# Kernel optimization log

Hardware: AMD Instinct MI355X
Metric: run time of the kernel (lower is better)

Reference implementation:

```python
import jax, jax.numpy as jnp
import numpy as np

D_LATENT = 8
N_CENTERS = 48
CHANNELS = 64
PM_STEPS = 4
DT, BETA, CLAMP = 0.12, 1.0, 3.0
SIGMA_E, SIGMA_I, K_E, K_I, GAIN = 0.6, 1.2, 0.8, 1.0, 0.06


def setup_inputs() -> dict:
    key = jax.random.key(0)
    ks = jax.random.split(key, 12)
    B = 8192
    x = jax.random.normal(ks[0], (B, 784), dtype=jnp.float32)
    # encoder params (torch Linear default-ish init scale)
    W1 = jax.random.normal(ks[1], (784, 256), dtype=jnp.float32) * (1.0 / np.sqrt(784))
    b1 = jnp.zeros((256,), jnp.float32)
    W2 = jax.random.normal(ks[2], (256, D_LATENT), dtype=jnp.float32) * (1.0 / np.sqrt(256))
    b2 = jnp.zeros((D_LATENT,), jnp.float32)
    centers = jax.random.normal(ks[3], (N_CENTERS, D_LATENT), dtype=jnp.float32) * 0.7
    mus = jnp.ones((N_CENTERS,), jnp.float32) * 0.4
    projW = jax.random.normal(ks[4], (D_LATENT, CHANNELS), dtype=jnp.float32) * (1.0 / np.sqrt(D_LATENT))
    projb = jnp.zeros((CHANNELS,), jnp.float32)
    roW = jax.random.normal(ks[5], (CHANNELS, 10), dtype=jnp.float32) * (1.0 / np.sqrt(CHANNELS))
    rob = jnp.zeros((10,), jnp.float32)
    return {"x": x, "W1": W1, "b1": b1, "W2": W2, "b2": b2,
            "centers": centers, "mus": mus, "projW": projW, "projb": projb,
            "roW": roW, "rob": rob, "T": 5}


def _pm_field(z, centers, mus):
    # one PMField forward: `PM_STEPS` gradient-flow steps on z [B, d]
    for _ in range(PM_STEPS):
        diff = z[:, None, :] - centers[None, :, :]            # [B, C, d]
        r2 = jnp.sum(diff * diff, axis=-1) + 1e-4              # [B, C]
        r = jnp.sqrt(r2)
        n = 1.0 + jnp.sum(mus[None, :] / r, axis=1)            # [B]
        g = -jnp.sum(mus[None, :, None] * diff / (r * r2)[:, :, None], axis=1)  # [B, d]
        z = z + DT * BETA * (g / n[:, None])
        z = jnp.clip(z, -CLAMP, CLAMP)
    return z


def _lateral_ei(z, h):
    # kernel computed with no_grad in torch -> stop_gradient here
    sq = jnp.sum(z * z, axis=1)                                # [B]
    dist2 = jnp.maximum(sq[:, None] + sq[None, :] - 2.0 * (z @ z.T), 0.0)
    Ke = K_E * jnp.exp(-dist2 / (2.0 * SIGMA_E ** 2))
    Ki = K_I * jnp.exp(-dist2 / (2.0 * SIGMA_I ** 2))
    K = Ke - Ki
    K = K / (jnp.sum(K, axis=1, keepdims=True) + 1e-6)
    K = jax.lax.stop_gradient(K)
    return GAIN * (K @ h)


def reference(x, W1, b1, W2, b2, centers, mus, projW, projb, roW, rob, T):
    z = jnp.tanh(x @ W1 + b1) @ W2 + b2                        # encoder -> [B, d]
    h = jnp.zeros((x.shape[0], CHANNELS), x.dtype)
    logits = None
    for _ in range(T):
        z = _pm_field(z, centers, mus)
        h = 0.9 * h + 0.1 * jnp.tanh(z @ projW + projb)
        h = h + _lateral_ei(z, h)
        logits = h @ roW + rob
    return logits, z, h
```

## Files before the change

kernel.cpp:

```cpp
#include <hip/hip_runtime.h>
#include <hip/hip_bf16.h>
#include <math.h>

#define B_N      8192
#define IN_DIM   784
#define HID      256
#define DL       8
#define NC       48
#define CH       64
#define NCLS     10
#define T_ITERS  5
#define TILES    128

#define DT_      0.12f
#define CLAMP_   3.0f
#define GAIN_    0.06f
#define SQIL2    0.70776814f
#define ONE_BF16 0x3F80u

#if defined(__has_builtin)
#if __has_builtin(__builtin_amdgcn_exp2f)
#define EXP2(x) __builtin_amdgcn_exp2f(x)
#endif
#endif
#ifndef EXP2
#define EXP2(x) exp2f(x)
#endif

typedef __attribute__((ext_vector_type(8))) short short8v;
typedef __attribute__((ext_vector_type(4))) float f32x4;

__device__ __forceinline__ unsigned int pack_bf16_rhu(float lo, float hi) {
    unsigned int b0 = __builtin_bit_cast(unsigned int, lo);
    unsigned int b1 = __builtin_bit_cast(unsigned int, hi);
    return ((b0 + 0x8000u) >> 16) | ((b1 + 0x8000u) & 0xFFFF0000u);
}
__device__ __forceinline__ unsigned short bf16_1(float x) {
    return (unsigned short)((__builtin_bit_cast(unsigned int, x) + 0x8000u) >> 16);
}
__device__ __forceinline__ float bf16_to_f(unsigned short h) {
    return __builtin_bit_cast(float, ((unsigned int)h) << 16);
}

__global__ __launch_bounds__(256) void k_gemm1_tanh(
    const float* __restrict__ x, const float* __restrict__ W1,
    const float* __restrict__ b1, float* __restrict__ H1)
{
    __shared__ float As[16][68];
    __shared__ float Bs[16][64];
    const int tid = threadIdx.x;
    const int row0 = blockIdx.x * 64;
    const int col0 = blockIdx.y * 64;
    const int tr = tid >> 4, tc = tid & 15;
    float acc[4][4] = {};
    for (int k0 = 0; k0 < IN_DIM; k0 += 16) {
        {
            int m = tid >> 2, kq = tid & 3;
            float4 v = *(const float4*)(x + (size_t)(row0 + m) * IN_DIM + k0 + kq * 4);
            As[kq*4+0][m] = v.x; As[kq*4+1][m] = v.y;
            As[kq*4+2][m] = v.z; As[kq*4+3][m] = v.w;
        }
        {
            int kk = tid >> 4, n4 = tid & 15;
            *(float4*)(&Bs[kk][n4*4]) =
                *(const float4*)(W1 + (size_t)(k0 + kk) * HID + col0 + n4 * 4);
        }
        __syncthreads();
        #pragma unroll
        for (int kk = 0; kk < 16; ++kk) {
            float4 a = *(const float4*)(&As[kk][tr*4]);
            float4 b = *(const float4*)(&Bs[kk][tc*4]);
            float av[4] = {a.x, a.y, a.z, a.w};
            float bv[4] = {b.x, b.y, b.z, b.w};
            #pragma unroll
            for (int i = 0; i < 4; ++i)
                #pragma unroll
                for (int j = 0; j < 4; ++j)
                    acc[i][j] += av[i] * bv[j];
        }
        __syncthreads();
    }
    #pragma unroll
    for (int i = 0; i < 4; ++i) {
        int r = row0 + tr*4 + i;
        #pragma unroll
        for (int j = 0; j < 4; ++j) {
            int c = col0 + tc*4 + j;
            H1[(size_t)r * HID + c] = tanhf(acc[i][j] + b1[c]);
        }
    }
}

__global__ __launch_bounds__(256) void k_gemm2(
    const float* __restrict__ H1, const float* __restrict__ W2,
    const float* __restrict__ b2, float* __restrict__ zbuf)
{
    __shared__ float W2s[HID][DL];
    const int tid = threadIdx.x;
    for (int l = tid; l < HID * DL; l += 256) W2s[l >> 3][l & 7] = W2[l];
    __syncthreads();
    const int row = blockIdx.x * 32 + (tid >> 3);
    const int d = tid & 7;
    float acc = b2[d];
    const float* hr = H1 + (size_t)row * HID;
    for (int k = 0; k < HID; k += 4) {
        float4 hv = *(const float4*)(hr + k);
        acc += hv.x * W2s[k][d] + hv.y * W2s[k+1][d]
             + hv.z * W2s[k+2][d] + hv.w * W2s[k+3][d];
    }
    zbuf[(size_t)row * DL + d] = acc;
}

template<int S, bool HP>
__global__ __launch_bounds__(256) void k_pm_proj(
    const float* __restrict__ centers, const float* __restrict__ mus,
    const float* __restrict__ projW, const float* __restrict__ projb,
    float* __restrict__ zbuf, float* __restrict__ hB,
    unsigned short* __restrict__ hTb,
    const float* __restrict__ pAcc, const float* __restrict__ pDen)
{
    __shared__ float4 cs4[NC][2];
    __shared__ float mu_s[NC];
    __shared__ float pW[DL][CH];
    __shared__ float pb[CH];
    const int tid = threadIdx.x;
    for (int l = tid; l < NC * 2; l += 256) cs4[l >> 1][l & 1] = ((const float4*)centers)[l];
    if (tid < NC) mu_s[tid] = mus[tid];
    for (int l = tid; l < DL * CH; l += 256) pW[l >> 6][l & 63] = projW[l];
    if (tid < CH) pb[tid] = projb[tid];
    __syncthreads();

    const int rloc = tid >> 3;
    const int dl = tid & 7;
    const int row = blockIdx.x * 32 + rloc;

    float4 cza[6], czb[6];
    float mur[6];
    #pragma unroll
    for (int k = 0; k < 6; ++k) {
        cza[k] = cs4[dl + 8*k][0];
        czb[k] = cs4[dl + 8*k][1];
        mur[k] = mu_s[dl + 8*k];
    }

    float z[8];
    {
        const float4* zp = (const float4*)(zbuf + (size_t)row * DL);
        float4 a = zp[0], b = zp[1];
        z[0]=a.x; z[1]=a.y; z[2]=a.z; z[3]=a.w;
        z[4]=b.x; z[5]=b.y; z[6]=b.z; z[7]=b.w;
    }

    #pragma unroll
    for (int step = 0; step < 4; ++step) {
        float np = 0.f;
        float gp[8] = {0,0,0,0,0,0,0,0};
        #pragma unroll
        for (int k = 0; k < 6; ++k) {
            float d0 = z[0]-cza[k].x, d1 = z[1]-cza[k].y;
            float d2 = z[2]-cza[k].z, d3 = z[3]-cza[k].w;
            float d4 = z[4]-czb[k].x, d5 = z[5]-czb[k].y;
            float d6 = z[6]-czb[k].z, d7 = z[7]-czb[k].w;
            float r2 = 1e-4f;
            r2 = fmaf(d0,d0,r2); r2 = fmaf(d1,d1,r2);
            r2 = fmaf(d2,d2,r2); r2 = fmaf(d3,d3,r2);
            r2 = fmaf(d4,d4,r2); r2 = fmaf(d5,d5,r2);
            r2 = fmaf(d6,d6,r2); r2 = fmaf(d7,d7,r2);
            float r = sqrtf(r2);
            float mr = mur[k] / r;
            np += mr;
            float t = mr / r2;
            gp[0] = fmaf(-t, d0, gp[0]); gp[1] = fmaf(-t, d1, gp[1]);
            gp[2] = fmaf(-t, d2, gp[2]); gp[3] = fmaf(-t, d3, gp[3]);
            gp[4] = fmaf(-t, d4, gp[4]); gp[5] = fmaf(-t, d5, gp[5]);
            gp[6] = fmaf(-t, d6, gp[6]); gp[7] = fmaf(-t, d7, gp[7]);
        }
        #pragma unroll
        for (int m = 1; m < 8; m <<= 1) {
            np += __shfl_xor(np, m);
            #pragma unroll
            for (int d = 0; d < 8; ++d) gp[d] += __shfl_xor(gp[d], m);
        }
        float s = DT_ / (1.f + np);
        #pragma unroll
        for (int d = 0; d < 8; ++d) {
            z[d] = fmaf(s, gp[d], z[d]);
            z[d] = fminf(fmaxf(z[d], -CLAMP_), CLAMP_);
        }
    }

    {
        float zout = z[0];
        #pragma unroll
        for (int d = 1; d < 8; ++d) zout = (dl == d) ? z[d] : zout;
        zbuf[(size_t)row * DL + dl] = zout;
    }

    const int c0 = dl * 8;
    float hin[8];
    if (HP) {
        float den = 1e-6f;
        #pragma unroll
        for (int s = 0; s < S; ++s) den += pDen[s * B_N + row];
        float inv = GAIN_ / den;
        #pragma unroll
        for (int q = 0; q < 2; ++q) {
            float4 a = {0.f, 0.f, 0.f, 0.f};
            #pragma unroll
            for (int s = 0; s < S; ++s) {
                float4 p = *(const float4*)(pAcc + (size_t)s * B_N * CH
                                            + (size_t)row * CH + c0 + q * 4);
                a.x += p.x; a.y += p.y; a.z += p.z; a.w += p.w;
            }
            float4 hm = *(const float4*)(hB + (size_t)row * CH + c0 + q * 4);
            hin[q*4+0] = fmaf(inv, a.x, hm.x);
            hin[q*4+1] = fmaf(inv, a.y, hm.y);
            hin[q*4+2] = fmaf(inv, a.z, hm.z);
            hin[q*4+3] = fmaf(inv, a.w, hm.w);
        }
    } else {
        #pragma unroll
        for (int k = 0; k < 8; ++k) hin[k] = 0.f;
    }
    #pragma unroll
    for (int k = 0; k < 8; ++k) {
        int c = c0 + k;
        float s = pb[c];
        #pragma unroll
        for (int dd = 0; dd < DL; ++dd) s = fmaf(z[dd], pW[dd][c], s);
        hin[k] = 0.9f * hin[k] + 0.1f * tanhf(s);
    }
    float4 o0 = {hin[0], hin[1], hin[2], hin[3]};
    float4 o1 = {hin[4], hin[5], hin[6], hin[7]};
    *(float4*)(hB + (size_t)row * CH + c0)     = o0;
    *(float4*)(hB + (size_t)row * CH + c0 + 4) = o1;

    {
        const int jl = row & 63;
        const int colp = (jl & 35) | ((jl & 12) << 1) | ((jl & 16) >> 2);
        const size_t tb = (size_t)(row & ~63) + colp;
        #pragma unroll
        for (int k = 0; k < 8; ++k)
            hTb[(size_t)(c0 + k) * B_N + tb] = bf16_1(hin[k]);
    }
}

template<int S>
__global__ __launch_bounds__(256, 4) void k_lateral(
    const float* __restrict__ zbuf, const unsigned short* __restrict__ hTb,
    float* __restrict__ pAcc, float* __restrict__ pDen)
{
    __shared__ __align__(16) unsigned short zA[2][64 * 24];
    __shared__ __align__(16) unsigned short hsT[2][CH][72];
    const int tid  = threadIdx.x;
    const int lane = tid & 63;
    const int wv   = tid >> 6;
    const int l15  = lane & 15;
    const int g    = lane >> 4;
    const int rowbase = blockIdx.x * 64;
    const int t0 = (TILES * blockIdx.y) / S;
    const int t1 = (TILES * (blockIdx.y + 1)) / S;
    const int chS = tid >> 2, segS = tid & 3;

    short8v bZ;
    {
        const int irow = rowbase + 16 * wv + l15;
        const float4* zp = (const float4*)(zbuf + (size_t)irow * DL);
        float4 a = zp[0], b = zp[1];
        float u[8] = {SQIL2*a.x, SQIL2*a.y, SQIL2*a.z, SQIL2*a.w,
                      SQIL2*b.x, SQIL2*b.y, SQIL2*b.z, SQIL2*b.w};
        float sq = 0.f;
        #pragma unroll
        for (int d = 0; d < 8; ++d) sq = fmaf(u[d], u[d], sq);
        float cin = -0.5f * sq;
        unsigned short hi[8]; float lo[8];
        #pragma unroll
        for (int d = 0; d < 8; ++d) {
            hi[d] = bf16_1(u[d]);
            lo[d] = u[d] - bf16_to_f(hi[d]);
        }
        unsigned short cih = bf16_1(cin);
        unsigned short cil = bf16_1(cin - bf16_to_f(cih));
        union { unsigned int u[4]; short8v v; } uh, ul, ua;
        #pragma unroll
        for (int d = 0; d < 4; ++d) {
            uh.u[d] = (unsigned int)hi[2*d] | ((unsigned int)hi[2*d+1] << 16);
            ul.u[d] = pack_bf16_rhu(lo[2*d], lo[2*d+1]);
        }
        ua.u[0] = ONE_BF16 | (ONE_BF16 << 16);
        ua.u[1] = (unsigned int)cih | ((unsigned int)cil << 16);
        ua.u[2] = 0; ua.u[3] = 0;
        bZ = (g == 2) ? ul.v : ((g == 3) ? ua.v : uh.v);
    }
    const int offsh = (g == 1) ? 8 : ((g == 3) ? 16 : 0);

    short8v bones;
    {
        union { unsigned int u[4]; short8v v; } uo;
        uo.u[0] = uo.u[1] = uo.u[2] = uo.u[3] = ONE_BF16 | (ONE_BF16 << 16);
        bones = uo.v;
    }

    f32x4 acc0 = {0,0,0,0}, acc1 = {0,0,0,0}, acc2 = {0,0,0,0}, acc3 = {0,0,0,0};
    f32x4 acc4 = {0,0,0,0};
    const f32x4 zc = {0,0,0,0};

    {
        const int jb = t0 * 64;
        if (tid < 64) {
            const float4* zp = (const float4*)(zbuf + (size_t)(jb + tid) * DL);
            float4 a = zp[0], b = zp[1];
            float u[8] = {SQIL2*a.x, SQIL2*a.y, SQIL2*a.z, SQIL2*a.w,
                          SQIL2*b.x, SQIL2*b.y, SQIL2*b.z, SQIL2*b.w};
            float sq = 0.f;
            #pragma unroll
            for (int d = 0; d < 8; ++d) sq = fmaf(u[d], u[d], sq);
            float cjn = -0.5f * sq;
            unsigned short hi[8]; float lo[8];
            #pragma unroll
            for (int d = 0; d < 8; ++d) {
                hi[d] = bf16_1(u[d]);
                lo[d] = u[d] - bf16_to_f(hi[d]);
            }
            unsigned short cjh = bf16_1(cjn);
            unsigned short cjl = bf16_1(cjn - bf16_to_f(cjh));
            uint4 W0, W1, W2;
            W0.x = (unsigned int)hi[0] | ((unsigned int)hi[1] << 16);
            W0.y = (unsigned int)hi[2] | ((unsigned int)hi[3] << 16);
            W0.z = (unsigned int)hi[4] | ((unsigned int)hi[5] << 16);
            W0.w = (unsigned int)hi[6] | ((unsigned int)hi[7] << 16);
            W1.x = pack_bf16_rhu(lo[0], lo[1]); W1.y = pack_bf16_rhu(lo[2], lo[3]);
            W1.z = pack_bf16_rhu(lo[4], lo[5]); W1.w = pack_bf16_rhu(lo[6], lo[7]);
            W2.x = (unsigned int)cjh | ((unsigned int)cjl << 16);
            W2.y = ONE_BF16 | (ONE_BF16 << 16);
            W2.z = 0; W2.w = 0;
            unsigned short* dst = &zA[0][tid * 24];
            *(uint4*)(dst)      = W0;
            *(uint4*)(dst + 8)  = W1;
            *(uint4*)(dst + 16) = W2;
        }
        const unsigned short* hs = hTb + (size_t)chS * B_N + jb + segS * 16;
        *(uint4*)(&hsT[0][chS][segS * 16])     = *(const uint4*)(hs);
        *(uint4*)(&hsT[0][chS][segS * 16 + 8]) = *(const uint4*)(hs + 8);
    }

    #pragma unroll 1
    for (int jt = t0; jt < t1; ++jt) {
        const int cur = (jt - t0) & 1;
        const bool more = (jt + 1 < t1);
        uint4 h0n, h1n;
        float4 zna, znb;
        if (more) {
            const int jb2 = (jt + 1) * 64;
            const unsigned short* hs = hTb + (size_t)chS * B_N + jb2 + segS * 16;
            h0n = *(const uint4*)(hs);
            h1n = *(const uint4*)(hs + 8);
            if (tid < 64) {
                const float4* zp = (const float4*)(zbuf + (size_t)(jb2 + tid) * DL);
                zna = zp[0]; znb = zp[1];
            }
        }
        __syncthreads();

        f32x4 gac[4];
        #pragma unroll
        for (int t = 0; t < 4; ++t) {
            short8v az = *(const short8v*)(&zA[cur][(t * 16 + l15) * 24 + offsh]);
            gac[t] = __builtin_amdgcn_mfma_f32_16x16x32_bf16(az, bZ, zc, 0, 0, 0);
        }

        short8v afr[2];
        #pragma unroll
        for (int kb = 0; kb < 2; ++kb) {
            float w8[8];
            #pragma unroll
            for (int m = 0; m < 8; ++m) {
                float out = gac[2 * kb + (m >> 2)][m & 3];
                float e1 = EXP2(out);
                float e2 = e1 * e1;
                float e4 = e2 * e2;
                float e8 = e4 * e4;
                w8[m] = fmaf(0.8f, e8, -e2);
            }
            union { unsigned int u[4]; short8v v; } uf;
            uf.u[0] = pack_bf16_rhu(w8[0], w8[1]);
            uf.u[1] = pack_bf16_rhu(w8[2], w8[3]);
            uf.u[2] = pack_bf16_rhu(w8[4], w8[5]);
            uf.u[3] = pack_bf16_rhu(w8[6], w8[7]);
            afr[kb] = uf.v;
        }

        #pragma unroll
        for (int kb = 0; kb < 2; ++kb) {
            const int jo = kb * 32 + g * 8;
            short8v b0 = *(const short8v*)&hsT[cur][ 0 + l15][jo];
            short8v b1 = *(const short8v*)&hsT[cur][16 + l15][jo];
            short8v b2 = *(const short8v*)&hsT[cur][32 + l15][jo];
            short8v b3 = *(const short8v*)&hsT[cur][48 + l15][jo];
            acc0 = __builtin_amdgcn_mfma_f32_16x16x32_bf16(afr[kb], b0, acc0, 0, 0, 0);
            acc1 = __builtin_amdgcn_mfma_f32_16x16x32_bf16(afr[kb], b1, acc1, 0, 0, 0);
            acc2 = __builtin_amdgcn_mfma_f32_16x16x32_bf16(afr[kb], b2, acc2, 0, 0, 0);
            acc3 = __builtin_amdgcn_mfma_f32_16x16x32_bf16(afr[kb], b3, acc3, 0, 0, 0);
            acc4 = __builtin_amdgcn_mfma_f32_16x16x32_bf16(afr[kb], bones, acc4, 0, 0, 0);
        }
        __syncthreads();

        if (more) {
            const int nb = cur ^ 1;
            if (tid < 64) {
                float u[8] = {SQIL2*zna.x, SQIL2*zna.y, SQIL2*zna.z, SQIL2*zna.w,
                              SQIL2*znb.x, SQIL2*znb.y, SQIL2*znb.z, SQIL2*znb.w};
                float sq = 0.f;
                #pragma unroll
                for (int d = 0; d < 8; ++d) sq = fmaf(u[d], u[d], sq);
                float cjn = -0.5f * sq;
                unsigned short hi[8]; float lo[8];
                #pragma unroll
                for (int d = 0; d < 8; ++d) {
                    hi[d] = bf16_1(u[d]);
                    lo[d] = u[d] - bf16_to_f(hi[d]);
                }
                unsigned short cjh = bf16_1(cjn);
                unsigned short cjl = bf16_1(cjn - bf16_to_f(cjh));
                uint4 W0, W1, W2;
                W0.x = (unsigned int)hi[0] | ((unsigned int)hi[1] << 16);
                W0.y = (unsigned int)hi[2] | ((unsigned int)hi[3] << 16);
                W0.z = (unsigned int)hi[4] | ((unsigned int)hi[5] << 16);
                W0.w = (unsigned int)hi[6] | ((unsigned int)hi[7] << 16);
                W1.x = pack_bf16_rhu(lo[0], lo[1]); W1.y = pack_bf16_rhu(lo[2], lo[3]);
                W1.z = pack_bf16_rhu(lo[4], lo[5]); W1.w = pack_bf16_rhu(lo[6], lo[7]);
                W2.x = (unsigned int)cjh | ((unsigned int)cjl << 16);
                W2.y = ONE_BF16 | (ONE_BF16 << 16);
                W2.z = 0; W2.w = 0;
                unsigned short* dst = &zA[nb][tid * 24];
                *(uint4*)(dst)      = W0;
                *(uint4*)(dst + 8)  = W1;
                *(uint4*)(dst + 16) = W2;
            }
            *(uint4*)(&hsT[nb][chS][segS * 16])     = h0n;
            *(uint4*)(&hsT[nb][chS][segS * 16 + 8]) = h1n;
        }
    }

    float* pA = pAcc + (size_t)blockIdx.y * (B_N * CH) + (size_t)rowbase * CH;
    #pragma unroll
    for (int r = 0; r < 4; ++r) {
        int gi = 16 * wv + g * 4 + r;
        pA[(size_t)gi * CH +  0 + l15] = acc0[r];
        pA[(size_t)gi * CH + 16 + l15] = acc1[r];
        pA[(size_t)gi * CH + 32 + l15] = acc2[r];
        pA[(size_t)gi * CH + 48 + l15] = acc3[r];
    }
    if (l15 == 0) {
        #pragma unroll
        for (int r = 0; r < 4; ++r)
            pDen[blockIdx.y * B_N + rowbase + 16 * wv + g * 4 + r] = acc4[r];
    }
}

template<int S>
__global__ __launch_bounds__(256) void k_logits_h(
    const float* __restrict__ hmid, const float* __restrict__ pAcc,
    const float* __restrict__ pDen, const float* __restrict__ roW,
    const float* __restrict__ rob, float* __restrict__ out_logits,
    float* __restrict__ out_h)
{
    __shared__ float hsh[64][68];
    __shared__ float ro[CH][NCLS];
    __shared__ float rb[NCLS];
    const int tid = threadIdx.x;
    for (int l = tid; l < CH * NCLS; l += 256) ro[l / NCLS][l % NCLS] = roW[l];
    if (tid < NCLS) rb[tid] = rob[tid];
    const int rowbase = blockIdx.x * 64;
    const int r  = tid >> 2;
    const int c0 = (tid & 3) * 16;
    const int row = rowbase + r;
    float den = 1e-6f;
    #pragma unroll
    for (int s = 0; s < S; ++s) den += pDen[s * B_N + row];
    float inv = GAIN_ / den;
    #pragma unroll
    for (int q = 0; q < 4; ++q) {
        float4 a = {0.f, 0.f, 0.f, 0.f};
        #pragma unroll
        for (int s = 0; s < S; ++s) {
            float4 p = *(const float4*)(pAcc + (size_t)s * B_N * CH
                                        + (size_t)row * CH + c0 + q * 4);
            a.x += p.x; a.y += p.y; a.z += p.z; a.w += p.w;
        }
        float4 hm = *(const float4*)(hmid + (size_t)row * CH + c0 + q * 4);
        float4 hv;
        hv.x = fmaf(inv, a.x, hm.x); hv.y = fmaf(inv, a.y, hm.y);
        hv.z = fmaf(inv, a.z, hm.z); hv.w = fmaf(inv, a.w, hm.w);
        *(float4*)(&hsh[r][c0 + q * 4]) = hv;
        *(float4*)(out_h + (size_t)row * CH + c0 + q * 4) = hv;
    }
    __syncthreads();
    for (int idx = tid; idx < 64 * NCLS; idx += 256) {
        int rr = idx / NCLS, o = idx % NCLS;
        float s = rb[o];
        #pragma unroll
        for (int k = 0; k < CH; ++k) s = fmaf(hsh[rr][k], ro[k][o], s);
        out_logits[(size_t)(rowbase + rr) * NCLS + o] = s;
    }
}

template<int S>
static void run_all(const float* x, const float* W1, const float* b1,
                    const float* W2, const float* b2, const float* centers,
                    const float* mus, const float* projW, const float* projb,
                    const float* roW, const float* rob,
                    float* ws, float* out, hipStream_t stream)
{
    float* pAcc = ws;
    float* pDen = ws + (size_t)S * B_N * CH;
    float* zbuf = pDen + (size_t)S * B_N;
    float* hB   = zbuf + B_N * DL;
    unsigned short* hTb = (unsigned short*)(hB + B_N * CH);
    float* H1   = ws;

    float* out_logits = out;
    float* out_z      = out + 81920;
    float* out_h      = out_z + 65536;

    k_gemm1_tanh<<<dim3(B_N / 64, HID / 64), 256, 0, stream>>>(x, W1, b1, H1);
    k_gemm2<<<B_N / 32, 256, 0, stream>>>(H1, W2, b2, zbuf);

    for (int t = 0; t < T_ITERS; ++t) {
        if (t == 0)
            k_pm_proj<S, false><<<B_N / 32, 256, 0, stream>>>(
                centers, mus, projW, projb, zbuf, hB, hTb, pAcc, pDen);
        else
            k_pm_proj<S, true><<<B_N / 32, 256, 0, stream>>>(
                centers, mus, projW, projb, zbuf, hB, hTb, pAcc, pDen);
        k_lateral<S><<<dim3(TILES, S), 256, 0, stream>>>(zbuf, hTb, pAcc, pDen);
    }

    k_logits_h<S><<<TILES, 256, 0, stream>>>(hB, pAcc, pDen, roW, rob,
                                             out_logits, out_h);
    hipMemcpyAsync(out_z, zbuf, (size_t)B_N * DL * sizeof(float),
                   hipMemcpyDeviceToDevice, stream);
}

extern "C" void kernel_launch(void* const* d_in, const int* in_sizes, int n_in,
                              void* d_out, int out_size, void* d_ws, size_t ws_size,
                              hipStream_t stream)
{
    const float* x       = (const float*)d_in[0];
    const float* W1      = (const float*)d_in[1];
    const float* b1      = (const float*)d_in[2];
    const float* W2      = (const float*)d_in[3];
    const float* b2      = (const float*)d_in[4];
    const float* centers = (const float*)d_in[5];
    const float* mus     = (const float*)d_in[6];
    const float* projW   = (const float*)d_in[7];
    const float* projb   = (const float*)d_in[8];
    const float* roW     = (const float*)d_in[9];
    const float* rob     = (const float*)d_in[10];

    float* ws  = (float*)d_ws;
    float* out = (float*)d_out;

    const size_t needS8 = ((size_t)8*B_N*CH + 8*B_N + B_N*DL + B_N*CH + B_N*CH/2) * 4;
    const size_t needS4 = ((size_t)4*B_N*CH + 4*B_N + B_N*DL + B_N*CH + B_N*CH/2) * 4;

    if (ws_size >= needS8)
        run_all<8>(x, W1, b1, W2, b2, centers, mus, projW, projb, roW, rob, ws, out, stream);
    else if (ws_size >= needS4)
        run_all<4>(x, W1, b1, W2, b2, centers, mus, projW, projb, roW, rob, ws, out, stream);
    else
        run_all<2>(x, W1, b1, W2, b2, centers, mus, projW, projb, roW, rob, ws, out, stream);
}
```

Baseline: 298.6 us.

## Give each lateral wave two row sets and shrink the encoder GEMM row tile

The lateral kernel now runs 128 threads (2 waves) per block, and each wave handles 32 rows as two 16-row sets. Each LDS fragment of the z and h tiles is therefore reused across two MFMA row sets, which halves LDS reads per MFMA but doubles accumulator registers per wave. Separately, the first encoder GEMM uses 32-row tiles with only half the threads loading A. That doubles the block count for better occupancy but lowers arithmetic intensity per thread. The repeated z bf16-splitting code is also factored into a helper.

```diff
diff --git a/kernel.cpp b/kernel.cpp
--- a/kernel.cpp
+++ b/kernel.cpp
@@ -42,19 +42,45 @@
     return __builtin_bit_cast(float, ((unsigned int)h) << 16);
 }
 
+__device__ __forceinline__ void z_split(const float4 a, const float4 b,
+                                        uint4& Whi, uint4& Wlo, unsigned int& Wc)
+{
+    float u[8] = {SQIL2*a.x, SQIL2*a.y, SQIL2*a.z, SQIL2*a.w,
+                  SQIL2*b.x, SQIL2*b.y, SQIL2*b.z, SQIL2*b.w};
+    float sq = 0.f;
+    #pragma unroll
+    for (int d = 0; d < 8; ++d) sq = fmaf(u[d], u[d], sq);
+    float cn = -0.5f * sq;
+    unsigned short hi[8]; float lo[8];
+    #pragma unroll
+    for (int d = 0; d < 8; ++d) {
+        hi[d] = bf16_1(u[d]);
+        lo[d] = u[d] - bf16_to_f(hi[d]);
+    }
+    unsigned short ch_ = bf16_1(cn);
+    unsigned short cl_ = bf16_1(cn - bf16_to_f(ch_));
+    Whi.x = (unsigned int)hi[0] | ((unsigned int)hi[1] << 16);
+    Whi.y = (unsigned int)hi[2] | ((unsigned int)hi[3] << 16);
+    Whi.z = (unsigned int)hi[4] | ((unsigned int)hi[5] << 16);
+    Whi.w = (unsigned int)hi[6] | ((unsigned int)hi[7] << 16);
+    Wlo.x = pack_bf16_rhu(lo[0], lo[1]); Wlo.y = pack_bf16_rhu(lo[2], lo[3]);
+    Wlo.z = pack_bf16_rhu(lo[4], lo[5]); Wlo.w = pack_bf16_rhu(lo[6], lo[7]);
+    Wc = (unsigned int)ch_ | ((unsigned int)cl_ << 16);
+}
+
 __global__ __launch_bounds__(256) void k_gemm1_tanh(
     const float* __restrict__ x, const float* __restrict__ W1,
     const float* __restrict__ b1, float* __restrict__ H1)
 {
-    __shared__ float As[16][68];
+    __shared__ float As[16][36];
     __shared__ float Bs[16][64];
     const int tid = threadIdx.x;
-    const int row0 = blockIdx.x * 64;
+    const int row0 = blockIdx.x * 32;
     const int col0 = blockIdx.y * 64;
     const int tr = tid >> 4, tc = tid & 15;
-    float acc[4][4] = {};
+    float acc[2][4] = {};
     for (int k0 = 0; k0 < IN_DIM; k0 += 16) {
-        {
+        if (tid < 128) {
             int m = tid >> 2, kq = tid & 3;
             float4 v = *(const float4*)(x + (size_t)(row0 + m) * IN_DIM + k0 + kq * 4);
             As[kq*4+0][m] = v.x; As[kq*4+1][m] = v.y;
@@ -68,21 +94,19 @@
         __syncthreads();
         #pragma unroll
         for (int kk = 0; kk < 16; ++kk) {
-            float4 a = *(const float4*)(&As[kk][tr*4]);
+            float a0 = As[kk][tr*2];
+            float a1 = As[kk][tr*2+1];
             float4 b = *(const float4*)(&Bs[kk][tc*4]);
-            float av[4] = {a.x, a.y, a.z, a.w};
-            float bv[4] = {b.x, b.y, b.z, b.w};
-            #pragma unroll
-            for (int i = 0; i < 4; ++i)
-                #pragma unroll
-                for (int j = 0; j < 4; ++j)
-                    acc[i][j] += av[i] * bv[j];
+            acc[0][0] += a0*b.x; acc[0][1] += a0*b.y;
+            acc[0][2] += a0*b.z; acc[0][3] += a0*b.w;
+            acc[1][0] += a1*b.x; acc[1][1] += a1*b.y;
+            acc[1][2] += a1*b.z; acc[1][3] += a1*b.w;
         }
         __syncthreads();
     }
     #pragma unroll
-    for (int i = 0; i < 4; ++i) {
-        int r = row0 + tr*4 + i;
+    for (int i = 0; i < 2; ++i) {
+        int r = row0 + tr*2 + i;
         #pragma unroll
         for (int j = 0; j < 4; ++j) {
             int c = col0 + tc*4 + j;
@@ -246,7 +270,7 @@
 }
 
 template<int S>
-__global__ __launch_bounds__(256, 4) void k_lateral(
+__global__ __launch_bounds__(128, 2) void k_lateral(
     const float* __restrict__ zbuf, const unsigned short* __restrict__ hTb,
     float* __restrict__ pAcc, float* __restrict__ pDen)
 {
@@ -260,37 +284,22 @@
     const int rowbase = blockIdx.x * 64;
     const int t0 = (TILES * blockIdx.y) / S;
     const int t1 = (TILES * (blockIdx.y + 1)) / S;
-    const int chS = tid >> 2, segS = tid & 3;
-
-    short8v bZ;
-    {
-        const int irow = rowbase + 16 * wv + l15;
+    const int chS = tid >> 1, hfS = tid & 1;
+
+    short8v bZa, bZb;
+    #pragma unroll
+    for (int setb = 0; setb < 2; ++setb) {
+        const int irow = rowbase + 32 * wv + 16 * setb + l15;
         const float4* zp = (const float4*)(zbuf + (size_t)irow * DL);
-        float4 a = zp[0], b = zp[1];
-        float u[8] = {SQIL2*a.x, SQIL2*a.y, SQIL2*a.z, SQIL2*a.w,
-                      SQIL2*b.x, SQIL2*b.y, SQIL2*b.z, SQIL2*b.w};
-        float sq = 0.f;
-        #pragma unroll
-        for (int d = 0; d < 8; ++d) sq = fmaf(u[d], u[d], sq);
-        float cin = -0.5f * sq;
-        unsigned short hi[8]; float lo[8];
-        #pragma unroll
-        for (int d = 0; d < 8; ++d) {
-            hi[d] = bf16_1(u[d]);
-            lo[d] = u[d] - bf16_to_f(hi[d]);
-        }
-        unsigned short cih = bf16_1(cin);
-        unsigned short cil = bf16_1(cin - bf16_to_f(cih));
+        uint4 Whi, Wlo; unsigned int Wc;
+        z_split(zp[0], zp[1], Whi, Wlo, Wc);
         union { unsigned int u[4]; short8v v; } uh, ul, ua;
-        #pragma unroll
-        for (int d = 0; d < 4; ++d) {
-            uh.u[d] = (unsigned int)hi[2*d] | ((unsigned int)hi[2*d+1] << 16);
-            ul.u[d] = pack_bf16_rhu(lo[2*d], lo[2*d+1]);
-        }
+        uh.u[0]=Whi.x; uh.u[1]=Whi.y; uh.u[2]=Whi.z; uh.u[3]=Whi.w;
+        ul.u[0]=Wlo.x; ul.u[1]=Wlo.y; ul.u[2]=Wlo.z; ul.u[3]=Wlo.w;
         ua.u[0] = ONE_BF16 | (ONE_BF16 << 16);
-        ua.u[1] = (unsigned int)cih | ((unsigned int)cil << 16);
-        ua.u[2] = 0; ua.u[3] = 0;
-        bZ = (g == 2) ? ul.v : ((g == 3) ? ua.v : uh.v);
+        ua.u[1] = Wc; ua.u[2] = 0; ua.u[3] = 0;
+        short8v bz = (g == 2) ? ul.v : ((g == 3) ? ua.v : uh.v);
+        if (setb == 0) bZa = bz; else bZb = bz;
     }
     const int offsh = (g == 1) ? 8 : ((g == 3) ? 16 : 0);
 
@@ -301,60 +310,44 @@
         bones = uo.v;
     }
 
-    f32x4 acc0 = {0,0,0,0}, acc1 = {0,0,0,0}, acc2 = {0,0,0,0}, acc3 = {0,0,0,0};
-    f32x4 acc4 = {0,0,0,0};
+    f32x4 accA0 = {0,0,0,0}, accA1 = {0,0,0,0}, accA2 = {0,0,0,0}, accA3 = {0,0,0,0};
+    f32x4 accB0 = {0,0,0,0}, accB1 = {0,0,0,0}, accB2 = {0,0,0,0}, accB3 = {0,0,0,0};
+    f32x4 acc4A = {0,0,0,0}, acc4B = {0,0,0,0};
     const f32x4 zc = {0,0,0,0};
 
     {
         const int jb = t0 * 64;
         if (tid < 64) {
             const float4* zp = (const float4*)(zbuf + (size_t)(jb + tid) * DL);
-            float4 a = zp[0], b = zp[1];
-            float u[8] = {SQIL2*a.x, SQIL2*a.y, SQIL2*a.z, SQIL2*a.w,
-                          SQIL2*b.x, SQIL2*b.y, SQIL2*b.z, SQIL2*b.w};
-            float sq = 0.f;
-            #pragma unroll
-            for (int d = 0; d < 8; ++d) sq = fmaf(u[d], u[d], sq);
-            float cjn = -0.5f * sq;
-            unsigned short hi[8]; float lo[8];
-            #pragma unroll
-            for (int d = 0; d < 8; ++d) {
-                hi[d] = bf16_1(u[d]);
-                lo[d] = u[d] - bf16_to_f(hi[d]);
-            }
-            unsigned short cjh = bf16_1(cjn);
-            unsigned short cjl = bf16_1(cjn - bf16_to_f(cjh));
-            uint4 W0, W1, W2;
-            W0.x = (unsigned int)hi[0] | ((unsigned int)hi[1] << 16);
-            W0.y = (unsigned int)hi[2] | ((unsigned int)hi[3] << 16);
-            W0.z = (unsigned int)hi[4] | ((unsigned int)hi[5] << 16);
-            W0.w = (unsigned int)hi[6] | ((unsigned int)hi[7] << 16);
-            W1.x = pack_bf16_rhu(lo[0], lo[1]); W1.y = pack_bf16_rhu(lo[2], lo[3]);
-            W1.z = pack_bf16_rhu(lo[4], lo[5]); W1.w = pack_bf16_rhu(lo[6], lo[7]);
-            W2.x = (unsigned int)cjh | ((unsigned int)cjl << 16);
-            W2.y = ONE_BF16 | (ONE_BF16 << 16);
-            W2.z = 0; W2.w = 0;
+            uint4 Whi, Wlo; unsigned int Wc;
+            z_split(zp[0], zp[1], Whi, Wlo, Wc);
+            uint4 W2v; W2v.x = Wc; W2v.y = ONE_BF16 | (ONE_BF16 << 16);
+            W2v.z = 0; W2v.w = 0;
             unsigned short* dst = &zA[0][tid * 24];
-            *(uint4*)(dst)      = W0;
-            *(uint4*)(dst + 8)  = W1;
-            *(uint4*)(dst + 16) = W2;
-        }
-        const unsigned short* hs = hTb + (size_t)chS * B_N + jb + segS * 16;
-        *(uint4*)(&hsT[0][chS][segS * 16])     = *(const uint4*)(hs);
-        *(uint4*)(&hsT[0][chS][segS * 16 + 8]) = *(const uint4*)(hs + 8);
+            *(uint4*)(dst)      = Whi;
+            *(uint4*)(dst + 8)  = Wlo;
+            *(uint4*)(dst + 16) = W2v;
+        }
+        const unsigned short* hs = hTb + (size_t)chS * B_N + jb + hfS * 32;
+        *(uint4*)(&hsT[0][chS][hfS*32])      = *(const uint4*)(hs);
+        *(uint4*)(&hsT[0][chS][hfS*32 + 8])  = *(const uint4*)(hs + 8);
+        *(uint4*)(&hsT[0][chS][hfS*32 + 16]) = *(const uint4*)(hs + 16);
+        *(uint4*)(&hsT[0][chS][hfS*32 + 24]) = *(const uint4*)(hs + 24);
     }
 
     #pragma unroll 1
     for (int jt = t0; jt < t1; ++jt) {
         const int cur = (jt - t0) & 1;
         const bool more = (jt + 1 < t1);
-        uint4 h0n, h1n;
+        uint4 h0n, h1n, h2n, h3n;
         float4 zna, znb;
         if (more) {
             const int jb2 = (jt + 1) * 64;
-            const unsigned short* hs = hTb + (size_t)chS * B_N + jb2 + segS * 16;
+            const unsigned short* hs = hTb + (size_t)chS * B_N + jb2 + hfS * 32;
             h0n = *(const uint4*)(hs);
             h1n = *(const uint4*)(hs + 8);
+            h2n = *(const uint4*)(hs + 16);
+            h3n = *(const uint4*)(hs + 24);
             if (tid < 64) {
                 const float4* zp = (const float4*)(zbuf + (size_t)(jb2 + tid) * DL);
                 zna = zp[0]; znb = zp[1];
@@ -362,20 +355,21 @@
         }
         __syncthreads();
 
-        f32x4 gac[4];
+        f32x4 gacA[4], gacB[4];
         #pragma unroll
         for (int t = 0; t < 4; ++t) {
             short8v az = *(const short8v*)(&zA[cur][(t * 16 + l15) * 24 + offsh]);
-            gac[t] = __builtin_amdgcn_mfma_f32_16x16x32_bf16(az, bZ, zc, 0, 0, 0);
-        }
-
-        short8v afr[2];
+            gacA[t] = __builtin_amdgcn_mfma_f32_16x16x32_bf16(az, bZa, zc, 0, 0, 0);
+            gacB[t] = __builtin_amdgcn_mfma_f32_16x16x32_bf16(az, bZb, zc, 0, 0, 0);
+        }
+
+        short8v afrA[2], afrB[2];
         #pragma unroll
         for (int kb = 0; kb < 2; ++kb) {
             float w8[8];
             #pragma unroll
             for (int m = 0; m < 8; ++m) {
-                float out = gac[2 * kb + (m >> 2)][m & 3];
+                float out = gacA[2 * kb + (m >> 2)][m & 3];
                 float e1 = EXP2(out);
                 float e2 = e1 * e1;
                 float e4 = e2 * e2;
@@ -387,7 +381,26 @@
             uf.u[1] = pack_bf16_rhu(w8[2], w8[3]);
             uf.u[2] = pack_bf16_rhu(w8[4], w8[5]);
             uf.u[3] = pack_bf16_rhu(w8[6], w8[7]);
-            afr[kb] = uf.v;
+            afrA[kb] = uf.v;
+        }
+        #pragma unroll
+        for (int kb = 0; kb < 2; ++kb) {
+            float w8[8];
+            #pragma unroll
+            for (int m = 0; m < 8; ++m) {
+                float out = gacB[2 * kb + (m >> 2)][m & 3];
+                float e1 = EXP2(out);
+                float e2 = e1 * e1;
+                float e4 = e2 * e2;
+                float e8 = e4 * e4;
+                w8[m] = fmaf(0.8f, e8, -e2);
+            }
+            union { unsigned int u[4]; short8v v; } uf;
+            uf.u[0] = pack_bf16_rhu(w8[0], w8[1]);
+            uf.u[1] = pack_bf16_rhu(w8[2], w8[3]);
+            uf.u[2] = pack_bf16_rhu(w8[4], w8[5]);
+            uf.u[3] = pack_bf16_rhu(w8[6], w8[7]);
+            afrB[kb] = uf.v;
         }
 
         #pragma unroll
@@ -397,64 +410,58 @@
             short8v b1 = *(const short8v*)&hsT[cur][16 + l15][jo];
             short8v b2 = *(const short8v*)&hsT[cur][32 + l15][jo];
             short8v b3 = *(const short8v*)&hsT[cur][48 + l15][jo];
-            acc0 = __builtin_amdgcn_mfma_f32_16x16x32_bf16(afr[kb], b0, acc0, 0, 0, 0);
-            acc1 = __builtin_amdgcn_mfma_f32_16x16x32_bf16(afr[kb], b1, acc1, 0, 0, 0);
-            acc2 = __builtin_amdgcn_mfma_f32_16x16x32_bf16(afr[kb], b2, acc2, 0, 0, 0);
-            acc3 = __builtin_amdgcn_mfma_f32_16x16x32_bf16(afr[kb], b3, acc3, 0, 0, 0);
-            acc4 = __builtin_amdgcn_mfma_f32_16x16x32_bf16(afr[kb], bones, acc4, 0, 0, 0);
+            accA0 = __builtin_amdgcn_mfma_f32_16x16x32_bf16(afrA[kb], b0, accA0, 0, 0, 0);
+            accA1 = __builtin_amdgcn_mfma_f32_16x16x32_bf16(afrA[kb], b1, accA1, 0, 0, 0);
+            accA2 = __builtin_amdgcn_mfma_f32_16x16x32_bf16(afrA[kb], b2, accA2, 0, 0, 0);
+            accA3 = __builtin_amdgcn_mfma_f32_16x16x32_bf16(afrA[kb], b3, accA3, 0, 0, 0);
+            accB0 = __builtin_amdgcn_mfma_f32_16x16x32_bf16(afrB[kb], b0, accB0, 0, 0, 0);
+            accB1 = __builtin_amdgcn_mfma_f32_16x16x32_bf16(afrB[kb], b1, accB1, 0, 0, 0);
+            accB2 = __builtin_amdgcn_mfma_f32_16x16x32_bf16(afrB[kb], b2, accB2, 0, 0, 0);
+            accB3 = __builtin_amdgcn_mfma_f32_16x16x32_bf16(afrB[kb], b3, accB3, 0, 0, 0);
+            acc4A = __builtin_amdgcn_mfma_f32_16x16x32_bf16(afrA[kb], bones, acc4A, 0, 0, 0);
+            acc4B = __builtin_amdgcn_mfma_f32_16x16x32_bf16(afrB[kb], bones, acc4B, 0, 0, 0);
         }
         __syncthreads();
 
         if (more) {
             const int nb = cur ^ 1;
             if (tid < 64) {
-                float u[8] = {SQIL2*zna.x, SQIL2*zna.y, SQIL2*zna.z, SQIL2*zna.w,
-                              SQIL2*znb.x, SQIL2*znb.y, SQIL2*znb.z, SQIL2*znb.w};
-                float sq = 0.f;
-                #pragma unroll
-                for (int d = 0; d < 8; ++d) sq = fmaf(u[d], u[d], sq);
-                float cjn = -0.5f * sq;
-                unsigned short hi[8]; float lo[8];
-                #pragma unroll
-                for (int d = 0; d < 8; ++d) {
-                    hi[d] = bf16_1(u[d]);
-                    lo[d] = u[d] - bf16_to_f(hi[d]);
-                }
-                unsigned short cjh = bf16_1(cjn);
-                unsigned short cjl = bf16_1(cjn - bf16_to_f(cjh));
-                uint4 W0, W1, W2;
-                W0.x = (unsigned int)hi[0] | ((unsigned int)hi[1] << 16);
-                W0.y = (unsigned int)hi[2] | ((unsigned int)hi[3] << 16);
-                W0.z = (unsigned int)hi[4] | ((unsigned int)hi[5] << 16);
-                W0.w = (unsigned int)hi[6] | ((unsigned int)hi[7] << 16);
-                W1.x = pack_bf16_rhu(lo[0], lo[1]); W1.y = pack_bf16_rhu(lo[2], lo[3]);
-                W1.z = pack_bf16_rhu(lo[4], lo[5]); W1.w = pack_bf16_rhu(lo[6], lo[7]);
-                W2.x = (unsigned int)cjh | ((unsigned int)cjl << 16);
-                W2.y = ONE_BF16 | (ONE_BF16 << 16);
-                W2.z = 0; W2.w = 0;
+                uint4 Whi, Wlo; unsigned int Wc;
+                z_split(zna, znb, Whi, Wlo, Wc);
+                uint4 W2v; W2v.x = Wc; W2v.y = ONE_BF16 | (ONE_BF16 << 16);
+                W2v.z = 0; W2v.w = 0;
                 unsigned short* dst = &zA[nb][tid * 24];
-                *(uint4*)(dst)      = W0;
-                *(uint4*)(dst + 8)  = W1;
-                *(uint4*)(dst + 16) = W2;
+                *(uint4*)(dst)      = Whi;
+                *(uint4*)(dst + 8)  = Wlo;
+                *(uint4*)(dst + 16) = W2v;
             }
-            *(uint4*)(&hsT[nb][chS][segS * 16])     = h0n;
-            *(uint4*)(&hsT[nb][chS][segS * 16 + 8]) = h1n;
+            *(uint4*)(&hsT[nb][chS][hfS*32])      = h0n;
+            *(uint4*)(&hsT[nb][chS][hfS*32 + 8])  = h1n;
+            *(uint4*)(&hsT[nb][chS][hfS*32 + 16]) = h2n;
+            *(uint4*)(&hsT[nb][chS][hfS*32 + 24]) = h3n;
         }
     }
 
     float* pA = pAcc + (size_t)blockIdx.y * (B_N * CH) + (size_t)rowbase * CH;
     #pragma unroll
     for (int r = 0; r < 4; ++r) {
-        int gi = 16 * wv + g * 4 + r;
-        pA[(size_t)gi * CH +  0 + l15] = acc0[r];
-        pA[(size_t)gi * CH + 16 + l15] = acc1[r];
-        pA[(size_t)gi * CH + 32 + l15] = acc2[r];
-        pA[(size_t)gi * CH + 48 + l15] = acc3[r];
+        int giA = 32 * wv + g * 4 + r;
+        int giB = giA + 16;
+        pA[(size_t)giA * CH +  0 + l15] = accA0[r];
+        pA[(size_t)giA * CH + 16 + l15] = accA1[r];
+        pA[(size_t)giA * CH + 32 + l15] = accA2[r];
+        pA[(size_t)giA * CH + 48 + l15] = accA3[r];
+        pA[(size_t)giB * CH +  0 + l15] = accB0[r];
+        pA[(size_t)giB * CH + 16 + l15] = accB1[r];
+        pA[(size_t)giB * CH + 32 + l15] = accB2[r];
+        pA[(size_t)giB * CH + 48 + l15] = accB3[r];
     }
     if (l15 == 0) {
         #pragma unroll
-        for (int r = 0; r < 4; ++r)
-            pDen[blockIdx.y * B_N + rowbase + 16 * wv + g * 4 + r] = acc4[r];
+        for (int r = 0; r < 4; ++r) {
+            pDen[blockIdx.y * B_N + rowbase + 32 * wv + g * 4 + r]      = acc4A[r];
+            pDen[blockIdx.y * B_N + rowbase + 32 * wv + 16 + g * 4 + r] = acc4B[r];
+        }
     }
 }
 
@@ -523,7 +530,7 @@
     float* out_z      = out + 81920;
     float* out_h      = out_z + 65536;
 
-    k_gemm1_tanh<<<dim3(B_N / 64, HID / 64), 256, 0, stream>>>(x, W1, b1, H1);
+    k_gemm1_tanh<<<dim3(B_N / 32, HID / 64), 256, 0, stream>>>(x, W1, b1, H1);
     k_gemm2<<<B_N / 32, 256, 0, stream>>>(H1, W2, b2, zbuf);
 
     for (int t = 0; t < T_ITERS; ++t) {
@@ -533,7 +540,7 @@
         else
             k_pm_proj<S, true><<<B_N / 32, 256, 0, stream>>>(
                 centers, mus, projW, projb, zbuf, hB, hTb, pAcc, pDen);
-        k_lateral<S><<<dim3(TILES, S), 256, 0, stream>>>(zbuf, hTb, pAcc, pDen);
+        k_lateral<S><<<dim3(TILES, S), 128, 0, stream>>>(zbuf, hTb, pAcc, pDen);
     }
 
     k_logits_h<S><<<TILES, 256, 0, stream>>>(hB, pAcc, pDen, roW, rob,
```

Result: slower. 328.8 us (+10.1%).
